# Kernel optimization log

Hardware: AMD Instinct MI355X
Metric: run time of the kernel (lower is better)

## Reference

```python
import jax, jax.numpy as jnp
import numpy as np


def setup_inputs() -> dict:
    key = jax.random.key(0)
    k1, k2, k3, k4, k5, k6 = jax.random.split(key, 6)
    Bsz, Cin, Cout, H, W = 8, 64, 64, 64, 64
    low_level_feat = jax.random.normal(k1, (Bsz, Cin, H, W), dtype=jnp.float32)
    high_level_feat = jax.random.normal(k2, (Bsz, Cin, H, W), dtype=jnp.float32)
    # 1x1 conv weights == per-pixel channel matmul
    W_low = jax.random.normal(k3, (Cout, Cin), dtype=jnp.float32) * (1.0 / np.sqrt(Cin))
    b_low = jax.random.normal(k4, (Cout,), dtype=jnp.float32) * 0.01
    W_high = jax.random.normal(k5, (Cout, Cin), dtype=jnp.float32) * (1.0 / np.sqrt(Cin))
    b_high = jax.random.normal(k6, (Cout,), dtype=jnp.float32) * 0.01
    return {
        "low_level_feat": low_level_feat,
        "high_level_feat": high_level_feat,
        "W_low": W_low,
        "b_low": b_low,
        "W_high": W_high,
        "b_high": b_high,
    }


def _conv1x1(x, W, b):
    # x: [B, Cin, H, W]; W: [Cout, Cin]; b: [Cout]
    return jnp.einsum('oi,bihw->bohw', W, x) + b[None, :, None, None]


def reference(low_level_feat, high_level_feat, W_low, b_low, W_high, b_high):
    A = _conv1x1(low_level_feat, W_low, b_low)          # [B, C, H, W]
    Bf = _conv1x1(high_level_feat, W_high, b_high)      # [B, C, H, W]
    Bsz, C, H, W = A.shape
    N = H * W
    P = A.reshape(Bsz, C, N)        # [B, C, N]
    Qf = Bf.reshape(Bsz, C, N)      # [B, C, N] (Q in torch is its transpose)
    # S[b,i,j] = sum_c Bf[b,c,i] * A[b,c,j]
    S = jnp.einsum('bci,bcj->bij', Qf, P)               # [B, N, N]
    S = jax.nn.softmax(S, axis=-1)
    # L[b,c,i] = sum_j Bf[b,c,j] * S[b,i,j]
    L = jnp.einsum('bcj,bij->bci', Qf, S)               # [B, C, N]
    O = Bf + L.reshape(Bsz, C, H, W)
    return O
```

## Files before the change

### kernel.cpp

```cpp
#include <hip/hip_runtime.h>
#include <hip/hip_bf16.h>
#include <stdint.h>

#define BATCH 8
#define NPOS 4096
#define LOG2E 1.4426950408889634f

typedef __attribute__((ext_vector_type(4)))  float f32x4;
typedef __attribute__((ext_vector_type(16))) float f32x16;
typedef __attribute__((ext_vector_type(8)))  short bf16x8;

#if __has_builtin(__builtin_amdgcn_exp2f)
#define EXP2(x) __builtin_amdgcn_exp2f(x)
#else
#define EXP2(x) exp2f(x)
#endif

#define SOFTMAX_FENCE() __builtin_amdgcn_sched_barrier(0x3F8)

__device__ __forceinline__ unsigned short bf_rne(float f) {
    unsigned u = __float_as_uint(f);
    u += 0x7fffu + ((u >> 16) & 1u);
    return (unsigned short)(u >> 16);
}
__device__ __forceinline__ unsigned cvt_pk_bf16(float lo, float hi) {
    unsigned r;
    asm("v_cvt_pk_bf16_f32 %0, %1, %2" : "=v"(r) : "v"(lo), "v"(hi));
    return r;
}
__device__ __forceinline__ void permswap32(unsigned &a, unsigned &b) {
    asm volatile("v_permlane32_swap_b32 %0, %1" : "+v"(a), "+v"(b));
}


__global__ __launch_bounds__(64)
void conv_prep(const float* __restrict__ xlow, const float* __restrict__ xhigh,
               const float* __restrict__ Wl, const float* __restrict__ bl,
               const float* __restrict__ Wh, const float* __restrict__ bh,
               unsigned short* __restrict__ KF, unsigned short* __restrict__ QThi,
               unsigned short* __restrict__ VF, float* __restrict__ R32)
{
    const int id   = blockIdx.x;
    const int b    = id & 7;
    const int rest = id >> 3;
    const int nb   = rest & 63;
    const int pass = (rest >> 6) & 1;
    const int oq   = rest >> 7;
    const int t    = threadIdx.x;
    const int n    = nb * 64 + t;
    const int o0   = oq * 16;

    const float* __restrict__ x    = pass ? xhigh : xlow;
    const float* __restrict__ W    = pass ? Wh : Wl;
    const float* __restrict__ bias = pass ? bh : bl;

    float xr[64];
#pragma unroll
    for (int i = 0; i < 64; ++i)
        xr[i] = x[((size_t)(b * 64 + i)) * NPOS + n];

    char* vbase = (char*)VF + ((size_t)b << 19) + nb * 8192 + ((t >> 5) & 1) * 4096
                + (oq >> 1) * 2048 + ((t >> 4) & 1) * 1024 + ((t >> 3) & 1) * 512
                + (oq & 1) * 256 + (t & 7) * 2;

    unsigned hpack[8];
#pragma unroll
    for (int oo = 0; oo < 16; ++oo) {
        const int o = o0 + oo;
        float acc = bias[o];
#pragma unroll
        for (int i = 0; i < 64; ++i)
            acc = fmaf(W[o * 64 + i], xr[i], acc);

        if (pass) {
            *(unsigned short*)(vbase + oo * 16) = bf_rne(acc);
            R32[((size_t)(b * 64 + o)) * NPOS + n] = acc;
        }
        unsigned short h = bf_rne(pass ? acc * LOG2E : acc);
        if (oo & 1) hpack[oo >> 1] |= ((unsigned)h) << 16;
        else        hpack[oo >> 1]  = h;
    }

    if (pass) {
        uint4* ph = (uint4*)(QThi + ((size_t)(b * NPOS + n)) * 64 + o0);
        uint4 v0; v0.x = hpack[0]; v0.y = hpack[1]; v0.z = hpack[2]; v0.w = hpack[3];
        uint4 v1; v1.x = hpack[4]; v1.y = hpack[5]; v1.z = hpack[6]; v1.w = hpack[7];
        ph[0] = v0; ph[1] = v1;
    } else {
        char* kbase = (char*)KF + ((size_t)b << 19) + nb * 8192 + ((t >> 5) & 1) * 4096
                    + oq * 1024 + (t & 31) * 16;
        uint4 v0; v0.x = hpack[0]; v0.y = hpack[1]; v0.z = hpack[2]; v0.w = hpack[3];
        uint4 v1; v1.x = hpack[4]; v1.y = hpack[5]; v1.z = hpack[6]; v1.w = hpack[7];
        *(uint4*)kbase         = v0;
        *(uint4*)(kbase + 512) = v1;
    }
}

__device__ __forceinline__ void stage_k(const unsigned short* __restrict__ KF,
                                        int b, int st, char* dst, int w, int lane)
{
    const char* src = (const char*)KF + ((size_t)b << 19) + (size_t)st * 8192
                    + w * 1024 + lane * 16;
    __builtin_amdgcn_global_load_lds(
        (const __attribute__((address_space(1))) unsigned int*)(const void*)src,
        (__attribute__((address_space(3))) unsigned int*)(void*)(dst + w * 1024),
        16, 0, 0);
}

__global__ __launch_bounds__(512, 4)
void attn_fused(const unsigned short* __restrict__ KF,
                const unsigned short* __restrict__ QThi,
                const unsigned short* __restrict__ VF,
                unsigned short* __restrict__ Pacc, float* __restrict__ Lp,
                int nsplit)
{
    const int id   = blockIdx.x;
    const int b    = id & 7;
    const int qb   = (id >> 3) & 15;
    const int s    = id >> 7;
    const int tid  = threadIdx.x;
    const int w    = tid >> 6;
    const int lane = tid & 63;
    const int r31  = lane & 31;
    const int g2   = lane >> 5;

    const int st0 = (64 * s) / nsplit;
    const int nst = (64 * (s + 1)) / nsplit - st0;

    __shared__ __align__(1024) char smem[16384];

    const int qrow = qb * 256 + w * 32 + r31;
    bf16x8 qhi[4];
#pragma unroll
    for (int kk = 0; kk < 4; ++kk)
        qhi[kk] = *(const bf16x8*)(QThi + ((size_t)b * NPOS + qrow) * 64 + kk * 16 + g2 * 8);

    f32x16 accO0, accO1;
#pragma unroll
    for (int r = 0; r < 16; ++r) { accO0[r] = 0.f; accO1[r] = 0.f; }
    float l_run = 0.f;

    stage_k(KF, b, st0, smem, w, lane);
    __syncthreads();

    for (int st = 0; st < nst; ++st) {
        char* buf = smem + (st & 1) * 8192;
        if (st + 1 < nst)
            stage_k(KF, b, st0 + st + 1, smem + ((st + 1) & 1) * 8192, w, lane);

#pragma unroll
        for (int itx = 0; itx < 2; ++itx) {
            const int it = itx ^ (w & 1);

            f32x16 sA;
#pragma unroll
            for (int r = 0; r < 16; ++r) sA[r] = 0.f;
            const char* Kb = buf + it * 4096;
            __builtin_amdgcn_s_setprio(1);
#pragma unroll
            for (int kk = 0; kk < 4; ++kk) {
                bf16x8 kh = *(const bf16x8*)(Kb + kk * 1024 + lane * 16);
                sA = __builtin_amdgcn_mfma_f32_32x32x16_bf16(kh, qhi[kk], sA, 0, 0, 0);
            }
            __builtin_amdgcn_s_setprio(0);

            const char* vbase = (const char*)VF + ((size_t)b << 19)
                              + (size_t)(st0 + st) * 8192 + it * 4096 + lane * 16;
            bf16x8 vf00 = *(const bf16x8*)(vbase);
            bf16x8 vf01 = *(const bf16x8*)(vbase + 1024);
            bf16x8 vf10 = *(const bf16x8*)(vbase + 2048);
            bf16x8 vf11 = *(const bf16x8*)(vbase + 3072);

            unsigned wpk[8];
            float lr0 = 0.f, lr1 = 0.f;
#pragma unroll
            for (int h = 0; h < 8; ++h) {
                float pa = EXP2(sA[2 * h]);
                float pb = EXP2(sA[2 * h + 1]);
                wpk[h] = cvt_pk_bf16(pa, pb);
                lr0 += pa;
                lr1 += pb;
                if (h & 1) SOFTMAX_FENCE();
            }
            l_run += lr0 + lr1;

            unsigned a0 = wpk[0], b0 = wpk[2]; permswap32(a0, b0);
            unsigned a1 = wpk[1], b1 = wpk[3]; permswap32(a1, b1);
            unsigned a2 = wpk[4], b2 = wpk[6]; permswap32(a2, b2);
            unsigned a3 = wpk[5], b3 = wpk[7]; permswap32(a3, b3);
            union { unsigned u[4]; bf16x8 v; } fa0, fa1;
            fa0.u[0] = a0; fa0.u[1] = a1; fa0.u[2] = b0; fa0.u[3] = b1;
            fa1.u[0] = a2; fa1.u[1] = a3; fa1.u[2] = b2; fa1.u[3] = b3;

            __builtin_amdgcn_s_setprio(1);
            accO0 = __builtin_amdgcn_mfma_f32_32x32x16_bf16(vf00, fa0.v, accO0, 0, 0, 0);
            accO0 = __builtin_amdgcn_mfma_f32_32x32x16_bf16(vf01, fa1.v, accO0, 0, 0, 0);
            accO1 = __builtin_amdgcn_mfma_f32_32x32x16_bf16(vf10, fa0.v, accO1, 0, 0, 0);
            accO1 = __builtin_amdgcn_mfma_f32_32x32x16_bf16(vf11, fa1.v, accO1, 0, 0, 0);
            __builtin_amdgcn_s_setprio(0);
        }
        __syncthreads();
    }

    const float l_tot = l_run + __shfl_xor(l_run, 32, 64);
#pragma unroll
    for (int r = 0; r < 16; ++r) {
        const int d0 = (r & 3) + 8 * (r >> 2) + 4 * g2;
        Pacc[(size_t)id * 16384 + (size_t)d0 * 256 + w * 32 + r31]        = bf_rne(accO0[r]);
        Pacc[(size_t)id * 16384 + (size_t)(d0 + 32) * 256 + w * 32 + r31] = bf_rne(accO1[r]);
    }
    if (g2 == 0)
        Lp[(size_t)id * 256 + w * 32 + r31] = l_tot;
}

__global__ __launch_bounds__(256)
void attn_combine(const unsigned short* __restrict__ Pacc, const float* __restrict__ Lp,
                  const float* __restrict__ R32, float* __restrict__ out, int nsplit)
{
    const int cid     = blockIdx.x;
    const int quarter = cid & 3;
    const int b       = (cid >> 2) & 7;
    const int qb      = cid >> 5;
    const int t       = threadIdx.x;

    __shared__ float invL[256];

    {
        float L = 0.f;
        for (int s = 0; s < nsplit; ++s)
            L += Lp[(size_t)((s << 7) | (qb << 3) | b) * 256 + t];
        invL[t] = 1.0f / L;
    }
    __syncthreads();

    const int c_loc = t >> 4;
    const int c     = quarter * 16 + c_loc;
    const int q0    = (t & 15) * 16;

    float acc[16];
#pragma unroll
    for (int i = 0; i < 16; ++i) acc[i] = 0.f;

    for (int s = 0; s < nsplit; ++s) {
        const size_t p = (size_t)((s << 7) | (qb << 3) | b);
        const bf16x8* pp = (const bf16x8*)(Pacc + p * 16384 + (size_t)c * 256 + q0);
#pragma unroll
        for (int h = 0; h < 2; ++h) {
            bf16x8 v = pp[h];
#pragma unroll
            for (int e = 0; e < 8; ++e)
                acc[h * 8 + e] += __uint_as_float(((unsigned)(unsigned short)v[e]) << 16);
        }
    }

    const size_t obase = ((size_t)(b * 64 + c)) * NPOS + qb * 256 + q0;
#pragma unroll
    for (int hv = 0; hv < 4; ++hv) {
        f32x4 rv = *(const f32x4*)(R32 + obase + hv * 4);
        f32x4 v;
#pragma unroll
        for (int e = 0; e < 4; ++e)
            v[e] = acc[hv * 4 + e] * invL[q0 + hv * 4 + e] + rv[e];
        *(f32x4*)(out + obase + hv * 4) = v;
    }
}

extern "C" void kernel_launch(void* const* d_in, const int* in_sizes, int n_in,
                              void* d_out, int out_size, void* d_ws, size_t ws_size,
                              hipStream_t stream)
{
    const float* xlow  = (const float*)d_in[0];
    const float* xhigh = (const float*)d_in[1];
    const float* Wl    = (const float*)d_in[2];
    const float* bl    = (const float*)d_in[3];
    const float* Wh    = (const float*)d_in[4];
    const float* bh    = (const float*)d_in[5];

    char* ws = (char*)d_ws;
    unsigned short* KF   = (unsigned short*)(ws);
    unsigned short* QThi = (unsigned short*)(ws + ( 4u << 20));
    unsigned short* VF   = (unsigned short*)(ws + ( 8u << 20));
    float*          R32  = (float*)         (ws + (12u << 20));

    const size_t base = (size_t)20u << 20;
    int nsplit = 4;
    while (nsplit > 1) {
        size_t nblk = (size_t)128 * nsplit;
        size_t need = base + nblk * 16384 * 2 + nblk * 256 * 4;
        if (need <= ws_size) break;
        nsplit >>= 1;
    }
    const size_t nblk = (size_t)128 * nsplit;
    unsigned short* Pacc = (unsigned short*)(ws + base);
    float*          Lp   = (float*)(ws + base + nblk * 16384 * 2);

    conv_prep<<<dim3(4096), dim3(64), 0, stream>>>(
        xlow, xhigh, Wl, bl, Wh, bh, KF, QThi, VF, R32);
    attn_fused<<<dim3((unsigned)nblk), dim3(512), 0, stream>>>(
        KF, QThi, VF, Pacc, Lp, nsplit);
    attn_combine<<<dim3(512), dim3(256), 0, stream>>>(
        Pacc, Lp, R32, (float*)d_out, nsplit);
}
```

Before: 76.37 us.

## Stage two K tiles per barrier and split conv prep into eight-channel blocks

The attention kernel now stages K tiles two at a time into a four-slot LDS ring (32 KB) and processes two tiles per __syncthreads, halving barriers and deepening prefetch. Separately, conv_prep computes 8 output channels per block instead of 16, doubling the grid to expose more parallelism at the cost of reloading inputs twice as often. Larger LDS may lower occupancy of the attention kernel, and the paired-step loop assumes an even tile count per split.

```diff
diff --git a/kernel.cpp b/kernel.cpp
--- a/kernel.cpp
+++ b/kernel.cpp
@@ -45,10 +45,10 @@
     const int rest = id >> 3;
     const int nb   = rest & 63;
     const int pass = (rest >> 6) & 1;
-    const int oq   = rest >> 7;
+    const int oe   = rest >> 7;
     const int t    = threadIdx.x;
     const int n    = nb * 64 + t;
-    const int o0   = oq * 16;
+    const int o0   = oe * 8;
 
     const float* __restrict__ x    = pass ? xhigh : xlow;
     const float* __restrict__ W    = pass ? Wh : Wl;
@@ -60,12 +60,12 @@
         xr[i] = x[((size_t)(b * 64 + i)) * NPOS + n];
 
     char* vbase = (char*)VF + ((size_t)b << 19) + nb * 8192 + ((t >> 5) & 1) * 4096
-                + (oq >> 1) * 2048 + ((t >> 4) & 1) * 1024 + ((t >> 3) & 1) * 512
-                + (oq & 1) * 256 + (t & 7) * 2;
-
-    unsigned hpack[8];
-#pragma unroll
-    for (int oo = 0; oo < 16; ++oo) {
+                + (oe >> 2) * 2048 + ((t >> 4) & 1) * 1024 + ((t >> 3) & 1) * 512
+                + (oe & 3) * 128 + (t & 7) * 2;
+
+    unsigned hpack[4];
+#pragma unroll
+    for (int oo = 0; oo < 8; ++oo) {
         const int o = o0 + oo;
         float acc = bias[o];
 #pragma unroll
@@ -81,18 +81,13 @@
         else        hpack[oo >> 1]  = h;
     }
 
+    uint4 v0; v0.x = hpack[0]; v0.y = hpack[1]; v0.z = hpack[2]; v0.w = hpack[3];
     if (pass) {
-        uint4* ph = (uint4*)(QThi + ((size_t)(b * NPOS + n)) * 64 + o0);
-        uint4 v0; v0.x = hpack[0]; v0.y = hpack[1]; v0.z = hpack[2]; v0.w = hpack[3];
-        uint4 v1; v1.x = hpack[4]; v1.y = hpack[5]; v1.z = hpack[6]; v1.w = hpack[7];
-        ph[0] = v0; ph[1] = v1;
+        *(uint4*)(QThi + ((size_t)(b * NPOS + n)) * 64 + o0) = v0;
     } else {
         char* kbase = (char*)KF + ((size_t)b << 19) + nb * 8192 + ((t >> 5) & 1) * 4096
-                    + oq * 1024 + (t & 31) * 16;
-        uint4 v0; v0.x = hpack[0]; v0.y = hpack[1]; v0.z = hpack[2]; v0.w = hpack[3];
-        uint4 v1; v1.x = hpack[4]; v1.y = hpack[5]; v1.z = hpack[6]; v1.w = hpack[7];
-        *(uint4*)kbase         = v0;
-        *(uint4*)(kbase + 512) = v1;
+                    + (oe >> 1) * 1024 + (oe & 1) * 512 + (t & 31) * 16;
+        *(uint4*)kbase = v0;
     }
 }
 
@@ -127,7 +122,7 @@
     const int st0 = (64 * s) / nsplit;
     const int nst = (64 * (s + 1)) / nsplit - st0;
 
-    __shared__ __align__(1024) char smem[16384];
+    __shared__ __align__(1024) char smem[32768];
 
     const int qrow = qb * 256 + w * 32 + r31;
     bf16x8 qhi[4];
@@ -140,64 +135,72 @@
     for (int r = 0; r < 16; ++r) { accO0[r] = 0.f; accO1[r] = 0.f; }
     float l_run = 0.f;
 
-    stage_k(KF, b, st0, smem, w, lane);
+    stage_k(KF, b, st0,     smem,        w, lane);
+    stage_k(KF, b, st0 + 1, smem + 8192, w, lane);
     __syncthreads();
 
-    for (int st = 0; st < nst; ++st) {
-        char* buf = smem + (st & 1) * 8192;
-        if (st + 1 < nst)
-            stage_k(KF, b, st0 + st + 1, smem + ((st + 1) & 1) * 8192, w, lane);
-
-#pragma unroll
-        for (int itx = 0; itx < 2; ++itx) {
-            const int it = itx ^ (w & 1);
-
-            f32x16 sA;
-#pragma unroll
-            for (int r = 0; r < 16; ++r) sA[r] = 0.f;
-            const char* Kb = buf + it * 4096;
-            __builtin_amdgcn_s_setprio(1);
-#pragma unroll
-            for (int kk = 0; kk < 4; ++kk) {
-                bf16x8 kh = *(const bf16x8*)(Kb + kk * 1024 + lane * 16);
-                sA = __builtin_amdgcn_mfma_f32_32x32x16_bf16(kh, qhi[kk], sA, 0, 0, 0);
+    for (int stp = 0; stp < nst; stp += 2) {
+        if (stp + 2 < nst) {
+            stage_k(KF, b, st0 + stp + 2, smem + ((stp + 2) & 3) * 8192, w, lane);
+            stage_k(KF, b, st0 + stp + 3, smem + ((stp + 3) & 3) * 8192, w, lane);
+        }
+
+#pragma unroll
+        for (int sub = 0; sub < 2; ++sub) {
+            const int st  = stp + sub;
+            char* buf = smem + (st & 3) * 8192;
+
+#pragma unroll
+            for (int itx = 0; itx < 2; ++itx) {
+                const int it = itx ^ (w & 1);
+
+                f32x16 sA;
+#pragma unroll
+                for (int r = 0; r < 16; ++r) sA[r] = 0.f;
+                const char* Kb = buf + it * 4096;
+                __builtin_amdgcn_s_setprio(1);
+#pragma unroll
+                for (int kk = 0; kk < 4; ++kk) {
+                    bf16x8 kh = *(const bf16x8*)(Kb + kk * 1024 + lane * 16);
+                    sA = __builtin_amdgcn_mfma_f32_32x32x16_bf16(kh, qhi[kk], sA, 0, 0, 0);
+                }
+                __builtin_amdgcn_s_setprio(0);
+
+                const char* vbase = (const char*)VF + ((size_t)b << 19)
+                                  + (size_t)(st0 + st) * 8192 + it * 4096 + lane * 16;
+                bf16x8 vf00 = *(const bf16x8*)(vbase);
+                bf16x8 vf01 = *(const bf16x8*)(vbase + 1024);
+                bf16x8 vf10 = *(const bf16x8*)(vbase + 2048);
+                bf16x8 vf11 = *(const bf16x8*)(vbase + 3072);
+
+                unsigned wpk[8];
+                float lr0 = 0.f, lr1 = 0.f;
+#pragma unroll
+                for (int h = 0; h < 8; ++h) {
+                    float pa = EXP2(sA[2 * h]);
+                    float pb = EXP2(sA[2 * h + 1]);
+                    wpk[h] = cvt_pk_bf16(pa, pb);
+                    lr0 += pa;
+                    lr1 += pb;
+                    if (h & 1) SOFTMAX_FENCE();
+                }
+                l_run += lr0 + lr1;
+
+                unsigned a0 = wpk[0], b0 = wpk[2]; permswap32(a0, b0);
+                unsigned a1 = wpk[1], b1 = wpk[3]; permswap32(a1, b1);
+                unsigned a2 = wpk[4], b2 = wpk[6]; permswap32(a2, b2);
+                unsigned a3 = wpk[5], b3 = wpk[7]; permswap32(a3, b3);
+                union { unsigned u[4]; bf16x8 v; } fa0, fa1;
+                fa0.u[0] = a0; fa0.u[1] = a1; fa0.u[2] = b0; fa0.u[3] = b1;
+                fa1.u[0] = a2; fa1.u[1] = a3; fa1.u[2] = b2; fa1.u[3] = b3;
+
+                __builtin_amdgcn_s_setprio(1);
+                accO0 = __builtin_amdgcn_mfma_f32_32x32x16_bf16(vf00, fa0.v, accO0, 0, 0, 0);
+                accO0 = __builtin_amdgcn_mfma_f32_32x32x16_bf16(vf01, fa1.v, accO0, 0, 0, 0);
+                accO1 = __builtin_amdgcn_mfma_f32_32x32x16_bf16(vf10, fa0.v, accO1, 0, 0, 0);
+                accO1 = __builtin_amdgcn_mfma_f32_32x32x16_bf16(vf11, fa1.v, accO1, 0, 0, 0);
+                __builtin_amdgcn_s_setprio(0);
             }
-            __builtin_amdgcn_s_setprio(0);
-
-            const char* vbase = (const char*)VF + ((size_t)b << 19)
-                              + (size_t)(st0 + st) * 8192 + it * 4096 + lane * 16;
-            bf16x8 vf00 = *(const bf16x8*)(vbase);
-            bf16x8 vf01 = *(const bf16x8*)(vbase + 1024);
-            bf16x8 vf10 = *(const bf16x8*)(vbase + 2048);
-            bf16x8 vf11 = *(const bf16x8*)(vbase + 3072);
-
-            unsigned wpk[8];
-            float lr0 = 0.f, lr1 = 0.f;
-#pragma unroll
-            for (int h = 0; h < 8; ++h) {
-                float pa = EXP2(sA[2 * h]);
-                float pb = EXP2(sA[2 * h + 1]);
-                wpk[h] = cvt_pk_bf16(pa, pb);
-                lr0 += pa;
-                lr1 += pb;
-                if (h & 1) SOFTMAX_FENCE();
-            }
-            l_run += lr0 + lr1;
-
-            unsigned a0 = wpk[0], b0 = wpk[2]; permswap32(a0, b0);
-            unsigned a1 = wpk[1], b1 = wpk[3]; permswap32(a1, b1);
-            unsigned a2 = wpk[4], b2 = wpk[6]; permswap32(a2, b2);
-            unsigned a3 = wpk[5], b3 = wpk[7]; permswap32(a3, b3);
-            union { unsigned u[4]; bf16x8 v; } fa0, fa1;
-            fa0.u[0] = a0; fa0.u[1] = a1; fa0.u[2] = b0; fa0.u[3] = b1;
-            fa1.u[0] = a2; fa1.u[1] = a3; fa1.u[2] = b2; fa1.u[3] = b3;
-
-            __builtin_amdgcn_s_setprio(1);
-            accO0 = __builtin_amdgcn_mfma_f32_32x32x16_bf16(vf00, fa0.v, accO0, 0, 0, 0);
-            accO0 = __builtin_amdgcn_mfma_f32_32x32x16_bf16(vf01, fa1.v, accO0, 0, 0, 0);
-            accO1 = __builtin_amdgcn_mfma_f32_32x32x16_bf16(vf10, fa0.v, accO1, 0, 0, 0);
-            accO1 = __builtin_amdgcn_mfma_f32_32x32x16_bf16(vf11, fa1.v, accO1, 0, 0, 0);
-            __builtin_amdgcn_s_setprio(0);
         }
         __syncthreads();
     }
@@ -294,7 +297,7 @@
     unsigned short* Pacc = (unsigned short*)(ws + base);
     float*          Lp   = (float*)(ws + base + nblk * 16384 * 2);
 
-    conv_prep<<<dim3(4096), dim3(64), 0, stream>>>(
+    conv_prep<<<dim3(8192), dim3(64), 0, stream>>>(
         xlow, xhigh, Wl, bl, Wh, bh, KF, QThi, VF, R32);
     attn_fused<<<dim3((unsigned)nblk), dim3(512), 0, stream>>>(
         KF, QThi, VF, Pacc, Lp, nsplit);
```

Result: slower. 78.90 us (+3.3%).
